# Optimization experiments

Hardware: AMD Instinct MI355X
Metric: run time of the kernel (lower is better)

## Reference

```python
import jax, jax.numpy as jnp
import numpy as np

IN_DIM, HIDDEN, CLASSES, NBASIS = 1024, 4096, 1000, 16

def setup_inputs() -> dict:
    key = jax.random.key(0)
    ks = jax.random.split(key, 7)
    x = jax.random.normal(ks[0], (4096, IN_DIM), dtype=jnp.float32)
    # FerroelectricBasis params: per-feature tanh basis (centers, scales) + dense mix
    centers = jax.random.normal(ks[1], (IN_DIM, NBASIS), dtype=jnp.float32)
    scales = jax.random.uniform(ks[2], (IN_DIM, NBASIS), dtype=jnp.float32, minval=0.5, maxval=2.0)
    s = 1.0 / np.sqrt(IN_DIM * NBASIS)
    Wb = jax.random.uniform(ks[3], (IN_DIM * NBASIS, HIDDEN), dtype=jnp.float32, minval=-s, maxval=s)
    bb = jax.random.uniform(ks[4], (HIDDEN,), dtype=jnp.float32, minval=-s, maxval=s)
    sh = 1.0 / np.sqrt(HIDDEN)
    Wh = jax.random.uniform(ks[5], (HIDDEN, CLASSES), dtype=jnp.float32, minval=-sh, maxval=sh)
    bh = jax.random.uniform(ks[6], (CLASSES,), dtype=jnp.float32, minval=-sh, maxval=sh)
    return {"x": x, "centers": centers, "scales": scales, "Wb": Wb, "bb": bb, "Wh": Wh, "bh": bh}

def reference(x, centers, scales, Wb, bb, Wh, bh):
    B = x.shape[0]
    # ferroelectric (hysteresis-like) tanh basis expansion: [B, in_dim, num_basis]
    feats = jnp.tanh((x[:, :, None] - centers[None]) * scales[None])
    feats = feats.reshape(B, -1)                      # [B, in_dim*num_basis]
    h = feats @ Wb + bb                               # [B, hidden]
    phi = jax.nn.sigmoid(h)
    logits = phi @ Wh + bh                            # [B, num_classes]
    return logits
```

## Files before the change

kernel.cpp:

```cpp
#include <hip/hip_runtime.h>
#include <hip/hip_bf16.h>

typedef __bf16 bf16x8_t __attribute__((ext_vector_type(8)));
typedef float f32x4_t __attribute__((ext_vector_type(4)));
typedef int i32x4_t __attribute__((ext_vector_type(4)));
typedef int i32x8_t __attribute__((ext_vector_type(8)));

#define GLDS(gp, lp) __builtin_amdgcn_global_load_lds(                        \
    (const __attribute__((address_space(1))) void*)(gp),                      \
    (__attribute__((address_space(3))) void*)(lp), 16, 0, 0)

__device__ __forceinline__ float fast_tanh(float z) {
  float zc = fminf(10.0f, fmaxf(-10.0f, z));
  float e = __expf(2.0f * zc);
  return 1.0f - 2.0f / (e + 1.0f);
}

__device__ __forceinline__ int pack_fp8x4(float a, float b, float c, float d) {
  int w = __builtin_amdgcn_cvt_pk_fp8_f32(a, b, 0, false);
  w = __builtin_amdgcn_cvt_pk_fp8_f32(c, d, w, true);
  return w;
}

__global__ __launch_bounds__(256) void feats_kernel(
    const float* __restrict__ x, const float* __restrict__ c,
    const float* __restrict__ s, unsigned char* __restrict__ out) {
  int idx = blockIdx.x * 256 + threadIdx.x;
  int d = idx & 1023;
  float xv = x[idx];
  const float4* c4 = (const float4*)(c + d * 16);
  const float4* s4 = (const float4*)(s + d * 16);
  int w[4];
#pragma unroll
  for (int g = 0; g < 4; ++g) {
    float4 cc = c4[g], ss = s4[g];
    float t0 = fast_tanh((xv - cc.x) * ss.x);
    float t1 = fast_tanh((xv - cc.y) * ss.y);
    float t2 = fast_tanh((xv - cc.z) * ss.z);
    float t3 = fast_tanh((xv - cc.w) * ss.w);
    w[g] = pack_fp8x4(t0, t1, t2, t3);
  }
  *(uint4*)(out + (size_t)idx * 16) = make_uint4(w[0], w[1], w[2], w[3]);
}

__global__ __launch_bounds__(256) void transpose_fp8(
    const float* __restrict__ src, unsigned char* __restrict__ dst, int R, int C) {
  __shared__ float tile[64][65];
  const int c0 = blockIdx.x * 64, r0 = blockIdx.y * 64;
  const int t = threadIdx.x;
  const int rr = t >> 4, cc4 = (t & 15) * 4;
#pragma unroll
  for (int p = 0; p < 4; ++p) {
    int row = rr + p * 16;
    float4 v = *(const float4*)(src + (size_t)(r0 + row) * C + c0 + cc4);
    tile[row][cc4 + 0] = v.x;
    tile[row][cc4 + 1] = v.y;
    tile[row][cc4 + 2] = v.z;
    tile[row][cc4 + 3] = v.w;
  }
  __syncthreads();
  const int drow = t >> 2, seg = (t & 3) * 16;
  int w[4];
#pragma unroll
  for (int g = 0; g < 4; ++g) {
    float a = tile[seg + g * 4 + 0][drow] * 128.0f;
    float b = tile[seg + g * 4 + 1][drow] * 128.0f;
    float cc = tile[seg + g * 4 + 2][drow] * 128.0f;
    float d = tile[seg + g * 4 + 3][drow] * 128.0f;
    w[g] = pack_fp8x4(a, b, cc, d);
  }
  *(uint4*)(dst + (size_t)(c0 + drow) * R + r0 + seg) = make_uint4(w[0], w[1], w[2], w[3]);
}

__global__ __launch_bounds__(256) void transpose_cast(
    const float* __restrict__ src, __hip_bfloat16* __restrict__ dst,
    int R, int C, int Cpad) {
  __shared__ float tile[64][65];
  const int c0 = blockIdx.x * 64, r0 = blockIdx.y * 64;
  const int t = threadIdx.x;
  const int rr = t >> 4, cc4 = (t & 15) * 4;
#pragma unroll
  for (int p = 0; p < 4; ++p) {
    int row = rr + p * 16;
    int cbase = c0 + cc4;
    float4 v;
    if (cbase + 3 < C) {
      v = *(const float4*)(src + (size_t)(r0 + row) * C + cbase);
    } else {
      v.x = (cbase + 0 < C) ? src[(size_t)(r0 + row) * C + cbase + 0] : 0.0f;
      v.y = (cbase + 1 < C) ? src[(size_t)(r0 + row) * C + cbase + 1] : 0.0f;
      v.z = (cbase + 2 < C) ? src[(size_t)(r0 + row) * C + cbase + 2] : 0.0f;
      v.w = (cbase + 3 < C) ? src[(size_t)(r0 + row) * C + cbase + 3] : 0.0f;
    }
    tile[row][cc4 + 0] = v.x;
    tile[row][cc4 + 1] = v.y;
    tile[row][cc4 + 2] = v.z;
    tile[row][cc4 + 3] = v.w;
  }
  __syncthreads();
#pragma unroll
  for (int p = 0; p < 2; ++p) {
    int i = t + 256 * p;
    int drow = i >> 3;
    int seg = (i & 7) * 8;
    int dc = c0 + drow;
    alignas(16) __hip_bfloat16 vals[8];
#pragma unroll
    for (int j = 0; j < 8; ++j) vals[j] = __float2bfloat16(tile[seg + j][drow]);
    if (dc < Cpad)
      *(uint4*)(dst + (size_t)dc * R + r0 + seg) = *(const uint4*)vals;
  }
}

__global__ __launch_bounds__(512, 2) void gemm1_mx8(
    const unsigned char* __restrict__ A, const unsigned char* __restrict__ Bt,
    const float* __restrict__ bias, __hip_bfloat16* __restrict__ outb,
    int M, int N, int K) {
  __shared__ unsigned char As[2][256 * 128];
  __shared__ unsigned char Bs[2][256 * 128];
  const int tid = threadIdx.x;
  const int wave = tid >> 6, lane = tid & 63;
  const int wm = (wave >> 2) * 128, wn = (wave & 3) * 64;

  const int bid = blockIdx.x;
  const int swz = (bid & 7) * 32 + (bid >> 3);
  const int gq = swz >> 5, u = swz & 31;
  const int gm0 = ((gq >> 1) * 4 + (u >> 3)) * 256;
  const int gn0 = ((gq & 1) * 8 + (u & 7)) * 256;

  const unsigned char* ga[4];
  const unsigned char* gb[4];
  int ldso[4];
#pragma unroll
  for (int p = 0; p < 4; ++p) {
    int c = p * 512 + tid;
    int row = c >> 3;
    int g = (c & 7) ^ (row & 7);
    ga[p] = A + (size_t)(gm0 + row) * K + g * 16;
    gb[p] = Bt + (size_t)(gn0 + row) * K + g * 16;
    ldso[p] = c * 16;
  }

  f32x4_t acc[8][4] = {};
  const int fr = lane & 15, kh = lane >> 4;

#pragma unroll
  for (int p = 0; p < 4; ++p) {
    GLDS(ga[p], &As[0][ldso[p]]);
    GLDS(gb[p], &Bs[0][ldso[p]]);
  }
  __syncthreads();

  const int NT = K >> 7;
  for (int t = 0; t < NT; ++t) {
    const unsigned char* Ac = As[t & 1];
    const unsigned char* Bc = Bs[t & 1];
    unsigned char* An = (unsigned char*)As[(t + 1) & 1];
    unsigned char* Bn = (unsigned char*)Bs[(t + 1) & 1];
    const int k1 = (t + 1) << 7;

    if (t + 1 < NT) {
#pragma unroll
      for (int p = 0; p < 4; ++p) {
        GLDS(ga[p] + k1, An + ldso[p]);
        GLDS(gb[p] + k1, Bn + ldso[p]);
      }
    }

    i32x8_t b[4];
#pragma unroll
    for (int j = 0; j < 4; ++j) {
      int rb = wn + j * 16 + fr, sb = rb & 7;
      i32x4_t blo = *(const i32x4_t*)(Bc + rb * 128 + (((2 * kh) ^ sb) * 16));
      i32x4_t bhi = *(const i32x4_t*)(Bc + rb * 128 + (((2 * kh + 1) ^ sb) * 16));
      b[j] = __builtin_shufflevector(blo, bhi, 0, 1, 2, 3, 4, 5, 6, 7);
    }

    __builtin_amdgcn_s_setprio(1);
#pragma unroll
    for (int i = 0; i < 8; ++i) {
      int ra = wm + i * 16 + fr, sa = ra & 7;
      i32x4_t lo = *(const i32x4_t*)(Ac + ra * 128 + (((2 * kh) ^ sa) * 16));
      i32x4_t hi = *(const i32x4_t*)(Ac + ra * 128 + (((2 * kh + 1) ^ sa) * 16));
      i32x8_t a = __builtin_shufflevector(lo, hi, 0, 1, 2, 3, 4, 5, 6, 7);
#pragma unroll
      for (int j = 0; j < 4; ++j)
        acc[i][j] = __builtin_amdgcn_mfma_scale_f32_16x16x128_f8f6f4(
            a, b[j], acc[i][j], 0, 0, 0, 0x7F7F7F7F, 0, 0x7F7F7F7F);
    }
    __builtin_amdgcn_s_setprio(0);
    __syncthreads();
  }

  const int cn = lane & 15, cm = (lane >> 4) * 4;
#pragma unroll
  for (int j = 0; j < 4; ++j) {
    int n = gn0 + wn + j * 16 + cn;
    float bv = bias[n];
#pragma unroll
    for (int i = 0; i < 8; ++i) {
#pragma unroll
      for (int r = 0; r < 4; ++r) {
        int m = gm0 + wm + i * 16 + cm + r;
        float v = acc[i][j][r] * 0.0078125f + bv;
        float phi = 1.0f / (1.0f + __expf(-v));
        outb[(size_t)m * N + n] = __float2bfloat16(phi);
      }
    }
  }
}

__global__ __launch_bounds__(256) void gemm2_full(
    const __hip_bfloat16* __restrict__ A, const __hip_bfloat16* __restrict__ Bt,
    const float* __restrict__ bh, float* __restrict__ out,
    int M, int N, int K) {
  __shared__ __hip_bfloat16 As[2][2][128 * 32];
  __shared__ __hip_bfloat16 Bs[2][2][128 * 32];
  const int tid = threadIdx.x;
  const int wave = tid >> 6, lane = tid & 63;
  const int wm = (wave >> 1) * 64, wn = (wave & 1) * 64;
  const int gm0 = blockIdx.y * 128, gn0 = blockIdx.x * 128;

  const int t1 = tid, t2 = tid + 256;
  const __hip_bfloat16* Ag0 = A + (size_t)(gm0 + (t1 >> 2)) * K + (t1 & 3) * 8;
  const __hip_bfloat16* Ag1 = A + (size_t)(gm0 + (t2 >> 2)) * K + (t2 & 3) * 8;
  const __hip_bfloat16* Bg0 = Bt + (size_t)(gn0 + (t1 >> 2)) * K + (t1 & 3) * 8;
  const __hip_bfloat16* Bg1 = Bt + (size_t)(gn0 + (t2 >> 2)) * K + (t2 & 3) * 8;

  f32x4_t acc[4][4] = {};
  const int fr = lane & 15, fk = (lane >> 4) * 8;

#pragma unroll
  for (int h = 0; h < 2; ++h) {
    GLDS(Ag0 + h * 32, &As[0][h][t1 * 8]);
    GLDS(Ag1 + h * 32, &As[0][h][t2 * 8]);
    GLDS(Bg0 + h * 32, &Bs[0][h][t1 * 8]);
    GLDS(Bg1 + h * 32, &Bs[0][h][t2 * 8]);
  }
  Ag0 += 64; Ag1 += 64; Bg0 += 64; Bg1 += 64;
  __syncthreads();

  const int nk = K >> 6;
  for (int it = 0; it < nk; ++it) {
    const int cur = it & 1;
    if (it + 1 < nk) {
      const int nxt = cur ^ 1;
#pragma unroll
      for (int h = 0; h < 2; ++h) {
        GLDS(Ag0 + h * 32, &As[nxt][h][t1 * 8]);
        GLDS(Ag1 + h * 32, &As[nxt][h][t2 * 8]);
        GLDS(Bg0 + h * 32, &Bs[nxt][h][t1 * 8]);
        GLDS(Bg1 + h * 32, &Bs[nxt][h][t2 * 8]);
      }
      Ag0 += 64; Ag1 += 64; Bg0 += 64; Bg1 += 64;
    }
#pragma unroll
    for (int h = 0; h < 2; ++h) {
      bf16x8_t a[4], b[4];
#pragma unroll
      for (int i = 0; i < 4; ++i) {
        a[i] = *(const bf16x8_t*)(&As[cur][h][(wm + i * 16 + fr) * 32 + fk]);
        b[i] = *(const bf16x8_t*)(&Bs[cur][h][(wn + i * 16 + fr) * 32 + fk]);
      }
#pragma unroll
      for (int i = 0; i < 4; ++i)
#pragma unroll
        for (int j = 0; j < 4; ++j)
          acc[i][j] = __builtin_amdgcn_mfma_f32_16x16x32_bf16(a[i], b[j], acc[i][j], 0, 0, 0);
    }
    __syncthreads();
  }

  const int cn = lane & 15, cm = (lane >> 4) * 4;
#pragma unroll
  for (int j = 0; j < 4; ++j) {
    int n = gn0 + wn + j * 16 + cn;
    if (n < 1000) {
      float bv = bh[n];
#pragma unroll
      for (int i = 0; i < 4; ++i)
#pragma unroll
        for (int r = 0; r < 4; ++r) {
          int m = gm0 + wm + i * 16 + cm + r;
          out[(size_t)m * 1000 + n] = acc[i][j][r] + bv;
        }
    }
  }
}

extern "C" void kernel_launch(void* const* d_in, const int* in_sizes, int n_in,
                              void* d_out, int out_size, void* d_ws, size_t ws_size,
                              hipStream_t stream) {
  const float* x = (const float*)d_in[0];
  const float* centers = (const float*)d_in[1];
  const float* scales = (const float*)d_in[2];
  const float* Wb = (const float*)d_in[3];
  const float* bb = (const float*)d_in[4];
  const float* Wh = (const float*)d_in[5];
  const float* bh = (const float*)d_in[6];
  float* out = (float*)d_out;

  unsigned char* feats = (unsigned char*)d_ws;
  unsigned char* Wbt = feats + (size_t)4096 * 16384;
  __hip_bfloat16* phi = (__hip_bfloat16*)(Wbt + (size_t)4096 * 16384);
  __hip_bfloat16* Wht = phi + (size_t)4096 * 4096;

  feats_kernel<<<dim3(16384), dim3(256), 0, stream>>>(x, centers, scales, feats);
  transpose_fp8<<<dim3(64, 256), dim3(256), 0, stream>>>(Wb, Wbt, 16384, 4096);
  transpose_cast<<<dim3(16, 64), dim3(256), 0, stream>>>(Wh, Wht, 4096, 1000, 1024);
  gemm1_mx8<<<dim3(256), dim3(512), 0, stream>>>(feats, Wbt, bb, phi, 4096, 4096, 16384);
  gemm2_full<<<dim3(8, 32), dim3(256), 0, stream>>>(phi, Wht, bh, out, 4096, 1024, 4096);
}
```

Baseline: 837.4 us.

## Switch FP8 GEMM1 to 32x32x64 MFMA with triple-buffered 64-wide K tiles

Rewrites the first GEMM to use the 32x32x64 scaled FP8 MFMA in place of 16x16x128. K tiles shrink to 64 bytes, with a new XOR swizzle for the narrower LDS rows. The shared-memory pipeline goes from double to triple buffering, using explicit vmcnt waits and a barrier so loads run two tiles ahead. The larger MFMA shape needs fewer LDS fragment reads per FLOP, and the deeper prefetch is meant to hide global latency. The trade-off is more loop iterations and barriers, plus a changed epilogue mapping for the 32x32 accumulator layout.

```diff
diff --git a/kernel.cpp b/kernel.cpp
--- a/kernel.cpp
+++ b/kernel.cpp
@@ -3,6 +3,7 @@
 
 typedef __bf16 bf16x8_t __attribute__((ext_vector_type(8)));
 typedef float f32x4_t __attribute__((ext_vector_type(4)));
+typedef float f32x16_t __attribute__((ext_vector_type(16)));
 typedef int i32x4_t __attribute__((ext_vector_type(4)));
 typedef int i32x8_t __attribute__((ext_vector_type(8)));
 
@@ -112,12 +113,12 @@
   }
 }
 
-__global__ __launch_bounds__(512, 2) void gemm1_mx8(
+__global__ __launch_bounds__(512, 2) void gemm1_mx32(
     const unsigned char* __restrict__ A, const unsigned char* __restrict__ Bt,
     const float* __restrict__ bias, __hip_bfloat16* __restrict__ outb,
     int M, int N, int K) {
-  __shared__ unsigned char As[2][256 * 128];
-  __shared__ unsigned char Bs[2][256 * 128];
+  __shared__ unsigned char As[3][256 * 64];
+  __shared__ unsigned char Bs[3][256 * 64];
   const int tid = threadIdx.x;
   const int wave = tid >> 6, lane = tid & 63;
   const int wm = (wave >> 2) * 128, wn = (wave & 3) * 64;
@@ -128,80 +129,90 @@
   const int gm0 = ((gq >> 1) * 4 + (u >> 3)) * 256;
   const int gn0 = ((gq & 1) * 8 + (u & 7)) * 256;
 
-  const unsigned char* ga[4];
-  const unsigned char* gb[4];
-  int ldso[4];
-#pragma unroll
-  for (int p = 0; p < 4; ++p) {
+  const unsigned char* ga[2];
+  const unsigned char* gb[2];
+  int ldso[2];
+#pragma unroll
+  for (int p = 0; p < 2; ++p) {
     int c = p * 512 + tid;
-    int row = c >> 3;
-    int g = (c & 7) ^ (row & 7);
+    int row = c >> 2;
+    int g = (c & 3) ^ ((row >> 1) & 3);
     ga[p] = A + (size_t)(gm0 + row) * K + g * 16;
     gb[p] = Bt + (size_t)(gn0 + row) * K + g * 16;
     ldso[p] = c * 16;
   }
 
-  f32x4_t acc[8][4] = {};
-  const int fr = lane & 15, kh = lane >> 4;
-
-#pragma unroll
-  for (int p = 0; p < 4; ++p) {
-    GLDS(ga[p], &As[0][ldso[p]]);
-    GLDS(gb[p], &Bs[0][ldso[p]]);
-  }
-  __syncthreads();
-
-  const int NT = K >> 7;
+  f32x16_t acc[4][2] = {};
+  const int fr = lane & 31, q = lane >> 5;
+
+  const int NT = K >> 6;
+#pragma unroll
+  for (int s = 0; s < 2; ++s) {
+#pragma unroll
+    for (int p = 0; p < 2; ++p) {
+      GLDS(ga[p] + s * 64, &As[s][ldso[p]]);
+      GLDS(gb[p] + s * 64, &Bs[s][ldso[p]]);
+    }
+  }
+
   for (int t = 0; t < NT; ++t) {
-    const unsigned char* Ac = As[t & 1];
-    const unsigned char* Bc = Bs[t & 1];
-    unsigned char* An = (unsigned char*)As[(t + 1) & 1];
-    unsigned char* Bn = (unsigned char*)Bs[(t + 1) & 1];
-    const int k1 = (t + 1) << 7;
-
     if (t + 1 < NT) {
-#pragma unroll
-      for (int p = 0; p < 4; ++p) {
-        GLDS(ga[p] + k1, An + ldso[p]);
-        GLDS(gb[p] + k1, Bn + ldso[p]);
+      asm volatile("s_waitcnt vmcnt(4)" ::: "memory");
+    } else {
+      asm volatile("s_waitcnt vmcnt(0)" ::: "memory");
+    }
+    __builtin_amdgcn_s_barrier();
+    __builtin_amdgcn_sched_barrier(0);
+
+    if (t + 2 < NT) {
+      unsigned char* An = (unsigned char*)As[(t + 2) % 3];
+      unsigned char* Bn = (unsigned char*)Bs[(t + 2) % 3];
+      const int ko = (t + 2) << 6;
+#pragma unroll
+      for (int p = 0; p < 2; ++p) {
+        GLDS(ga[p] + ko, An + ldso[p]);
+        GLDS(gb[p] + ko, Bn + ldso[p]);
       }
     }
 
-    i32x8_t b[4];
-#pragma unroll
-    for (int j = 0; j < 4; ++j) {
-      int rb = wn + j * 16 + fr, sb = rb & 7;
-      i32x4_t blo = *(const i32x4_t*)(Bc + rb * 128 + (((2 * kh) ^ sb) * 16));
-      i32x4_t bhi = *(const i32x4_t*)(Bc + rb * 128 + (((2 * kh + 1) ^ sb) * 16));
-      b[j] = __builtin_shufflevector(blo, bhi, 0, 1, 2, 3, 4, 5, 6, 7);
-    }
-
-    __builtin_amdgcn_s_setprio(1);
-#pragma unroll
-    for (int i = 0; i < 8; ++i) {
-      int ra = wm + i * 16 + fr, sa = ra & 7;
-      i32x4_t lo = *(const i32x4_t*)(Ac + ra * 128 + (((2 * kh) ^ sa) * 16));
-      i32x4_t hi = *(const i32x4_t*)(Ac + ra * 128 + (((2 * kh + 1) ^ sa) * 16));
+    const unsigned char* Ac = As[t % 3];
+    const unsigned char* Bc = Bs[t % 3];
+
+    i32x8_t b[2];
+#pragma unroll
+    for (int j = 0; j < 2; ++j) {
+      int rb = wn + j * 32 + fr;
+      int f = (rb >> 1) & 3;
+      i32x4_t lo = *(const i32x4_t*)(Bc + rb * 64 + (((2 * q) ^ f) * 16));
+      i32x4_t hi = *(const i32x4_t*)(Bc + rb * 64 + (((2 * q + 1) ^ f) * 16));
+      b[j] = __builtin_shufflevector(lo, hi, 0, 1, 2, 3, 4, 5, 6, 7);
+    }
+#pragma unroll
+    for (int i = 0; i < 4; ++i) {
+      int ra = wm + i * 32 + fr;
+      int f = (ra >> 1) & 3;
+      i32x4_t lo = *(const i32x4_t*)(Ac + ra * 64 + (((2 * q) ^ f) * 16));
+      i32x4_t hi = *(const i32x4_t*)(Ac + ra * 64 + (((2 * q + 1) ^ f) * 16));
       i32x8_t a = __builtin_shufflevector(lo, hi, 0, 1, 2, 3, 4, 5, 6, 7);
-#pragma unroll
-      for (int j = 0; j < 4; ++j)
-        acc[i][j] = __builtin_amdgcn_mfma_scale_f32_16x16x128_f8f6f4(
-            a, b[j], acc[i][j], 0, 0, 0, 0x7F7F7F7F, 0, 0x7F7F7F7F);
-    }
-    __builtin_amdgcn_s_setprio(0);
-    __syncthreads();
-  }
-
-  const int cn = lane & 15, cm = (lane >> 4) * 4;
-#pragma unroll
-  for (int j = 0; j < 4; ++j) {
-    int n = gn0 + wn + j * 16 + cn;
+      __builtin_amdgcn_s_setprio(1);
+      acc[i][0] = __builtin_amdgcn_mfma_scale_f32_32x32x64_f8f6f4(
+          a, b[0], acc[i][0], 0, 0, 0, 0x7F7F7F7F, 0, 0x7F7F7F7F);
+      acc[i][1] = __builtin_amdgcn_mfma_scale_f32_32x32x64_f8f6f4(
+          a, b[1], acc[i][1], 0, 0, 0, 0x7F7F7F7F, 0, 0x7F7F7F7F);
+      __builtin_amdgcn_s_setprio(0);
+    }
+  }
+
+  const int cn = lane & 31, cq = lane >> 5;
+#pragma unroll
+  for (int j = 0; j < 2; ++j) {
+    int n = gn0 + wn + j * 32 + cn;
     float bv = bias[n];
 #pragma unroll
-    for (int i = 0; i < 8; ++i) {
-#pragma unroll
-      for (int r = 0; r < 4; ++r) {
-        int m = gm0 + wm + i * 16 + cm + r;
+    for (int i = 0; i < 4; ++i) {
+#pragma unroll
+      for (int r = 0; r < 16; ++r) {
+        int m = gm0 + wm + i * 32 + (r & 3) + 8 * (r >> 2) + 4 * cq;
         float v = acc[i][j][r] * 0.0078125f + bv;
         float phi = 1.0f / (1.0f + __expf(-v));
         outb[(size_t)m * N + n] = __float2bfloat16(phi);
@@ -308,6 +319,6 @@
   feats_kernel<<<dim3(16384), dim3(256), 0, stream>>>(x, centers, scales, feats);
   transpose_fp8<<<dim3(64, 256), dim3(256), 0, stream>>>(Wb, Wbt, 16384, 4096);
   transpose_cast<<<dim3(16, 64), dim3(256), 0, stream>>>(Wh, Wht, 4096, 1000, 1024);
-  gemm1_mx8<<<dim3(256), dim3(512), 0, stream>>>(feats, Wbt, bb, phi, 4096, 4096, 16384);
+  gemm1_mx32<<<dim3(256), dim3(512), 0, stream>>>(feats, Wbt, bb, phi, 4096, 4096, 16384);
   gemm2_full<<<dim3(8, 32), dim3(256), 0, stream>>>(phi, Wht, bh, out, 4096, 1024, 4096);
 }
```

Measured after the change: 882.3 us. +5.4%, slower.

## Use partial vmcnt waits and split barriers to overlap prefetch with MFMA

Applied to the files above, without the earlier changes.

Replaces the full __syncthreads after issuing next-tile global-to-LDS loads with an explicit s_waitcnt vmcnt(8), so only the current tile's loads must land while the prefetch stays in flight. The fp8 GEMM's MFMA loop is also regrouped into pairs of A rows, with s_barrier between groups to interleave the waves' LDS reads and MFMA issue. The aim is to stop draining all outstanding memory ops every iteration. The cost is correctness that depends on the exact count of outstanding loads and on barrier semantics across waves.

```diff
diff --git a/kernel.cpp b/kernel.cpp
--- a/kernel.cpp
+++ b/kernel.cpp
@@ -149,23 +149,27 @@
     GLDS(ga[p], &As[0][ldso[p]]);
     GLDS(gb[p], &Bs[0][ldso[p]]);
   }
-  __syncthreads();
 
   const int NT = K >> 7;
   for (int t = 0; t < NT; ++t) {
     const unsigned char* Ac = As[t & 1];
     const unsigned char* Bc = Bs[t & 1];
-    unsigned char* An = (unsigned char*)As[(t + 1) & 1];
-    unsigned char* Bn = (unsigned char*)Bs[(t + 1) & 1];
-    const int k1 = (t + 1) << 7;
 
     if (t + 1 < NT) {
+      unsigned char* An = (unsigned char*)As[(t + 1) & 1];
+      unsigned char* Bn = (unsigned char*)Bs[(t + 1) & 1];
+      const int k1 = (t + 1) << 7;
 #pragma unroll
       for (int p = 0; p < 4; ++p) {
         GLDS(ga[p] + k1, An + ldso[p]);
         GLDS(gb[p] + k1, Bn + ldso[p]);
       }
-    }
+      asm volatile("s_waitcnt vmcnt(8)" ::: "memory");
+    } else {
+      asm volatile("s_waitcnt vmcnt(0)" ::: "memory");
+    }
+    __builtin_amdgcn_s_barrier();
+    __builtin_amdgcn_sched_barrier(0);
 
     i32x8_t b[4];
 #pragma unroll
@@ -176,20 +180,33 @@
       b[j] = __builtin_shufflevector(blo, bhi, 0, 1, 2, 3, 4, 5, 6, 7);
     }
 
-    __builtin_amdgcn_s_setprio(1);
-#pragma unroll
-    for (int i = 0; i < 8; ++i) {
-      int ra = wm + i * 16 + fr, sa = ra & 7;
-      i32x4_t lo = *(const i32x4_t*)(Ac + ra * 128 + (((2 * kh) ^ sa) * 16));
-      i32x4_t hi = *(const i32x4_t*)(Ac + ra * 128 + (((2 * kh + 1) ^ sa) * 16));
-      i32x8_t a = __builtin_shufflevector(lo, hi, 0, 1, 2, 3, 4, 5, 6, 7);
-#pragma unroll
-      for (int j = 0; j < 4; ++j)
-        acc[i][j] = __builtin_amdgcn_mfma_scale_f32_16x16x128_f8f6f4(
-            a, b[j], acc[i][j], 0, 0, 0, 0x7F7F7F7F, 0, 0x7F7F7F7F);
-    }
-    __builtin_amdgcn_s_setprio(0);
-    __syncthreads();
+#pragma unroll
+    for (int p = 0; p < 4; ++p) {
+      i32x8_t a0, a1;
+      {
+        int ra = wm + (2 * p + 0) * 16 + fr, sa = ra & 7;
+        i32x4_t lo = *(const i32x4_t*)(Ac + ra * 128 + (((2 * kh) ^ sa) * 16));
+        i32x4_t hi = *(const i32x4_t*)(Ac + ra * 128 + (((2 * kh + 1) ^ sa) * 16));
+        a0 = __builtin_shufflevector(lo, hi, 0, 1, 2, 3, 4, 5, 6, 7);
+      }
+      {
+        int ra = wm + (2 * p + 1) * 16 + fr, sa = ra & 7;
+        i32x4_t lo = *(const i32x4_t*)(Ac + ra * 128 + (((2 * kh) ^ sa) * 16));
+        i32x4_t hi = *(const i32x4_t*)(Ac + ra * 128 + (((2 * kh + 1) ^ sa) * 16));
+        a1 = __builtin_shufflevector(lo, hi, 0, 1, 2, 3, 4, 5, 6, 7);
+      }
+      __builtin_amdgcn_s_barrier();
+      __builtin_amdgcn_s_setprio(1);
+#pragma unroll
+      for (int j = 0; j < 4; ++j) {
+        acc[2 * p + 0][j] = __builtin_amdgcn_mfma_scale_f32_16x16x128_f8f6f4(
+            a0, b[j], acc[2 * p + 0][j], 0, 0, 0, 0x7F7F7F7F, 0, 0x7F7F7F7F);
+        acc[2 * p + 1][j] = __builtin_amdgcn_mfma_scale_f32_16x16x128_f8f6f4(
+            a1, b[j], acc[2 * p + 1][j], 0, 0, 0, 0x7F7F7F7F, 0, 0x7F7F7F7F);
+      }
+      __builtin_amdgcn_s_setprio(0);
+    }
+    __builtin_amdgcn_s_barrier();
   }
 
   const int cn = lane & 15, cm = (lane >> 4) * 4;
@@ -238,7 +255,6 @@
     GLDS(Bg1 + h * 32, &Bs[0][h][t2 * 8]);
   }
   Ag0 += 64; Ag1 += 64; Bg0 += 64; Bg1 += 64;
-  __syncthreads();
 
   const int nk = K >> 6;
   for (int it = 0; it < nk; ++it) {
@@ -253,7 +269,12 @@
         GLDS(Bg1 + h * 32, &Bs[nxt][h][t2 * 8]);
       }
       Ag0 += 64; Ag1 += 64; Bg0 += 64; Bg1 += 64;
-    }
+      asm volatile("s_waitcnt vmcnt(8)" ::: "memory");
+    } else {
+      asm volatile("s_waitcnt vmcnt(0)" ::: "memory");
+    }
+    __builtin_amdgcn_s_barrier();
+    __builtin_amdgcn_sched_barrier(0);
 #pragma unroll
     for (int h = 0; h < 2; ++h) {
       bf16x8_t a[4], b[4];
@@ -268,7 +289,7 @@
         for (int j = 0; j < 4; ++j)
           acc[i][j] = __builtin_amdgcn_mfma_f32_16x16x32_bf16(a[i], b[j], acc[i][j], 0, 0, 0);
     }
-    __syncthreads();
+    __builtin_amdgcn_s_barrier();
   }
 
   const int cn = lane & 15, cm = (lane >> 4) * 4;
```

New measurement: 873.1 us. 4.3% more time.
